# Optimization experiments

Hardware: AMD Instinct MI355X
Metric: run time of the kernel (lower is better)

Reference implementation:

```python
import jax, jax.numpy as jnp
import numpy as np

N_NODES = 100_000
N_EDGES = 1_600_000
IN_FEAT = 128
N_HEADS = 8
OUT_FEAT = 16
HF = N_HEADS * OUT_FEAT  # 128
NEG_SLOPE = 0.2


def setup_inputs() -> dict:
    key = jax.random.key(0)
    k = jax.random.split(key, 9)
    x = jax.random.normal(k[0], (N_NODES, IN_FEAT), dtype=jnp.float32)
    src = jax.random.randint(k[1], (N_EDGES,), 0, N_NODES, dtype=jnp.int64)
    dst = jax.random.randint(k[2], (N_EDGES,), 0, N_NODES, dtype=jnp.int64)
    sv = 1.0 / np.sqrt(IN_FEAT)
    sa = 1.0 / np.sqrt(HF)
    Wv = jax.random.normal(k[3], (IN_FEAT, HF), dtype=jnp.float32) * sv
    bv = jnp.zeros((HF,), dtype=jnp.float32)
    Wq = jax.random.normal(k[4], (HF, N_HEADS), dtype=jnp.float32) * sa
    bq = jnp.zeros((N_HEADS,), dtype=jnp.float32)
    Wk = jax.random.normal(k[5], (HF, N_HEADS), dtype=jnp.float32) * sa
    bk = jnp.zeros((N_HEADS,), dtype=jnp.float32)
    return {"x": x, "src": src, "dst": dst, "Wv": Wv, "bv": bv,
            "Wq": Wq, "bq": bq, "Wk": Wk, "bk": bk}


def reference(x, src, dst, Wv, bv, Wq, bq, Wk, bk):
    # Dense projections (homogeneous graph: h_src == h_dst == h)
    h = x @ Wv + bv                       # [N, H*F]
    q = h @ Wq + bq                       # [N, H]  (query, attached via dst)
    k = h @ Wk + bk                       # [N, H]  (key, attached via src)
    u = h.reshape(N_NODES, N_HEADS, OUT_FEAT)  # [N, H, F]

    # Edge scores: u_add_v('k','q') -> e_ij = k[src] + q[dst], then leaky-relu
    e = k[src] + q[dst]                   # [E, H]
    coeff = jnp.where(e >= 0, e, NEG_SLOPE * e)

    # Segment softmax over incoming edges of each destination node
    seg_max = jax.ops.segment_max(coeff, dst, num_segments=N_NODES)   # [N, H]
    ex = jnp.exp(coeff - seg_max[dst])                                # [E, H]
    denom = jax.ops.segment_sum(ex, dst, num_segments=N_NODES)       # [N, H]
    attn = ex / denom[dst]                                           # [E, H]

    # Weighted message + scatter-sum aggregate
    m = u[src] * attn[:, :, None]                                    # [E, H, F]
    v = jax.ops.segment_sum(m, dst, num_segments=N_NODES)            # [N, H, F]

    return jnp.mean(v, axis=1)                                       # [N, F]
```

## Files before the change

### kernel.cpp

```cpp
#include <hip/hip_runtime.h>
#include <hip/hip_fp16.h>

#define NFEAT 128
#define NHEADS 8
#define OUTF 16
#define NPB 256
#define MAXNB 512
#define CAP 4736

typedef _Float16 half8 __attribute__((ext_vector_type(8)));
typedef float float4v __attribute__((ext_vector_type(4)));

__global__ __launch_bounds__(256) void prep_kernel(
    const float* __restrict__ Wv, const float* __restrict__ bv,
    const float* __restrict__ Wq, const float* __restrict__ bq,
    const float* __restrict__ Wk, const float* __restrict__ bk,
    float* __restrict__ Wvq, float* __restrict__ Wvk,
    float* __restrict__ bq2, float* __restrict__ bk2)
{
    const int t = threadIdx.x;
    const int idx = blockIdx.x * 256 + t;
    const int m  = idx >> 10;
    const int j  = (idx >> 3) & 127;
    const int hd = idx & 7;
    const float* w = m ? Wk : Wq;
    float acc = 0.f;
#pragma unroll 8
    for (int c = 0; c < NFEAT; c++) acc += Wv[j * NFEAT + c] * w[c * NHEADS + hd];
    if (m) Wvk[j * NHEADS + hd] = acc;
    else   Wvq[j * NHEADS + hd] = acc;

    if (blockIdx.x == 0 && t < 16) {
        int mm = t >> 3, hh = t & 7;
        const float* ww = mm ? Wk : Wq;
        float a = mm ? bk[hh] : bq[hh];
        for (int c = 0; c < NFEAT; c++) a += bv[c] * ww[c * NHEADS + hh];
        if (mm) bk2[hh] = a;
        else    bq2[hh] = a;
    }
}

__global__ __launch_bounds__(256) void gemm_h_kernel(
    const float* __restrict__ x, const float* __restrict__ Wv,
    const float* __restrict__ bv, const float* __restrict__ Wvq,
    const float* __restrict__ Wvk, const float* __restrict__ bq2,
    const float* __restrict__ bk2, __half* __restrict__ h,
    float* __restrict__ qarr, float* __restrict__ karr, int M)
{
    __shared__ _Float16 sw[144][136];
    const int t = threadIdx.x;

    for (int i = t; i < 128 * 128; i += 256) {
        int k = i >> 7, n = i & 127;
        sw[n][k] = (_Float16)Wv[i];
    }
    for (int i = t; i < 128 * 16; i += 256) {
        int k = i >> 4, o = i & 15;
        float v = (o < 8) ? Wvq[k * 8 + o] : Wvk[k * 8 + (o - 8)];
        sw[128 + o][k] = (_Float16)v;
    }
    __syncthreads();

    const int wave = t >> 6, lane = t & 63;
    const int quad = lane >> 4, l16 = lane & 15;
    const int nstrips = (M + 15) >> 4;

    float bvv[8];
#pragma unroll
    for (int tl = 0; tl < 8; tl++) bvv[tl] = bv[tl * 16 + l16];
    const float qb = (l16 < 8) ? bq2[l16] : bk2[l16 - 8];

#pragma unroll
    for (int s = 0; s < 2; s++) {
        const int strip = blockIdx.x * 8 + wave + s * 4;
        if (strip >= nstrips) break;
        const int row0 = strip * 16;
        const int xr = row0 + l16;
        const bool ok = (xr < M);
        const float* xp = x + (size_t)xr * NFEAT + quad * 8;

        half8 af[4];
#pragma unroll
        for (int kc = 0; kc < 4; kc++) {
            float4 f0 = make_float4(0.f, 0.f, 0.f, 0.f);
            float4 f1 = make_float4(0.f, 0.f, 0.f, 0.f);
            if (ok) {
                f0 = *(const float4*)(xp + kc * 32);
                f1 = *(const float4*)(xp + kc * 32 + 4);
            }
            half8 a;
            a[0] = (_Float16)f0.x; a[1] = (_Float16)f0.y;
            a[2] = (_Float16)f0.z; a[3] = (_Float16)f0.w;
            a[4] = (_Float16)f1.x; a[5] = (_Float16)f1.y;
            a[6] = (_Float16)f1.z; a[7] = (_Float16)f1.w;
            af[kc] = a;
        }

        float4v acc[9];
#pragma unroll
        for (int tl = 0; tl < 9; tl++) acc[tl] = (float4v){0.f, 0.f, 0.f, 0.f};

#pragma unroll
        for (int kc = 0; kc < 4; kc++) {
#pragma unroll
            for (int tl = 0; tl < 9; tl++) {
                half8 b = *(const half8*)&sw[tl * 16 + l16][kc * 32 + quad * 8];
                acc[tl] = __builtin_amdgcn_mfma_f32_16x16x32_f16(af[kc], b, acc[tl], 0, 0, 0);
            }
        }

#pragma unroll
        for (int r = 0; r < 4; r++) {
            int row = row0 + quad * 4 + r;
            if (row < M) {
#pragma unroll
                for (int tl = 0; tl < 8; tl++)
                    h[(size_t)row * NFEAT + tl * 16 + l16] =
                        __float2half(acc[tl][r] + bvv[tl]);
                float qv = acc[8][r] + qb;
                if (l16 < 8) qarr[(size_t)row * NHEADS + l16] = qv;
                else         karr[(size_t)row * NHEADS + (l16 - 8)] = qv;
            }
        }
    }
}

__global__ __launch_bounds__(1024) void bin_kernel(
    const int* __restrict__ src, const int* __restrict__ dst,
    int* __restrict__ tail, int* __restrict__ bin, int E, int NB)
{
    __shared__ int lcnt[MAXNB];
    __shared__ int lbase[MAXNB];
    const int t = threadIdx.x;
    const int e0 = blockIdx.x * 8192;

    for (int i = t; i < NB; i += 1024) lcnt[i] = 0;
    __syncthreads();

    int pack[8], bkt[8], rank[8];
#pragma unroll
    for (int k = 0; k < 8; k++) {
        int e = e0 + k * 1024 + t;
        bkt[k] = -1;
        if (e < E) {
            int d = dst[e];
            pack[k] = (src[e] << 8) | (d & (NPB - 1));
            bkt[k]  = d >> 8;
            rank[k] = atomicAdd(&lcnt[bkt[k]], 1);
        }
    }
    __syncthreads();
    for (int i = t; i < NB; i += 1024)
        lbase[i] = lcnt[i] ? atomicAdd(&tail[i], lcnt[i]) : 0;
    __syncthreads();

#pragma unroll
    for (int k = 0; k < 8; k++) {
        if (bkt[k] >= 0) {
            int pos = lbase[bkt[k]] + rank[k];
            if (pos < CAP) bin[(size_t)bkt[k] * CAP + pos] = pack[k];
        }
    }
}

__global__ __launch_bounds__(1024) void bucket_build_kernel(
    const int* __restrict__ bin, const int* __restrict__ tail,
    int* __restrict__ deg, int* __restrict__ off,
    int* __restrict__ csr, int N, int NB)
{
    __shared__ int stail[MAXNB];
    __shared__ int lcnt[NPB];
    __shared__ int lcur[NPB];
    __shared__ int lcsr[CAP];

    const int b = blockIdx.x;
    const int t = threadIdx.x;

    for (int i = t; i < MAXNB; i += 1024) stail[i] = (i < NB) ? tail[i] : 0;
    if (t < NPB) lcnt[t] = 0;
    __syncthreads();

    for (int o = 1; o < MAXNB; o <<= 1) {
        int u = (t < MAXNB && t >= o) ? stail[t - o] : 0;
        __syncthreads();
        if (t < MAXNB) stail[t] += u;
        __syncthreads();
    }
    const int gbase = (b > 0) ? stail[b - 1] : 0;
    const int cnt = min(tail[b], CAP);
    const int n0 = b << 8;
    const int* mybin = bin + (size_t)b * CAP;

    for (int i = t; i < cnt; i += 1024) atomicAdd(&lcnt[mybin[i] & (NPB - 1)], 1);
    __syncthreads();

    if (t < NPB) lcur[t] = lcnt[t];
    __syncthreads();
    for (int o = 1; o < NPB; o <<= 1) {
        int u = (t < NPB && t >= o) ? lcur[t - o] : 0;
        __syncthreads();
        if (t < NPB) lcur[t] += u;
        __syncthreads();
    }
    if (t < NPB) {
        int excl = lcur[t] - lcnt[t];
        lcur[t] = excl;
        int node = n0 + t;
        if (node < N) {
            deg[node] = lcnt[t];
            off[node] = gbase + excl;
        }
    }
    __syncthreads();

    for (int i = t; i < cnt; i += 1024) {
        int p = mybin[i];
        int r = atomicAdd(&lcur[p & (NPB - 1)], 1);
        lcsr[r] = p >> 8;
    }
    __syncthreads();

    for (int i = t; i < cnt; i += 1024) csr[gbase + i] = lcsr[i];
}

__global__ __launch_bounds__(256) void agg_kernel(
    const int* __restrict__ csr, const int* __restrict__ off,
    const int* __restrict__ deg, const float* __restrict__ karr,
    const float* __restrict__ qarr, const __half* __restrict__ h,
    float* __restrict__ out, int nnodes)
{
    const int wave = threadIdx.x >> 6;
    const int lane = threadIdx.x & 63;
    const int d = blockIdx.x * 4 + wave;
    if (d >= nnodes) return;

    const int dg = deg[d];
    const int o0 = off[d];
    const int h8  = lane & 7;
    const int eg  = lane >> 4;
    const int l16 = lane & 15;
    const int hd  = l16 >> 1;
    const float q1 = qarr[d * NHEADS + h8];
    const __half* hbase = h + l16 * 8;

    __half2 acc0 = __float2half2_rn(0.f);
    __half2 acc1 = __float2half2_rn(0.f);
    __half2 acc2 = __float2half2_rn(0.f);
    __half2 acc3 = __float2half2_rn(0.f);
    float den8 = 0.f;

    for (int c0 = 0; c0 < dg; c0 += 64) {
        const int cnt = min(64, dg - c0);
        int sv = (lane < cnt) ? csr[o0 + c0 + lane] : 0;
        for (int g0 = 0; g0 < cnt; g0 += 8) {
            const int epos = g0 + (lane >> 3);
            int s8 = __shfl(sv, epos, 64);
            float p = 0.f;
            if (epos < cnt) {
                float c = karr[s8 * NHEADS + h8] + q1;
                c = fmaxf(c, 0.2f * c);
                p = __expf(c) * 0.0009765625f;
            }
            den8 += p;
            __half2 ph2 = __half2half2(__float2half(p));
            int phi = *(int*)&ph2;
#pragma unroll
            for (int i = 0; i < 2; ++i) {
                int jr  = (i << 2) + eg;
                int sl  = __shfl(sv, g0 + jr, 64);
                int pw  = __shfl(phi, (jr << 3) + hd, 64);
                __half2 pv = *(__half2*)&pw;
                float4 raw = *(const float4*)(hbase + (size_t)sl * NFEAT);
                __half2 v0 = *(__half2*)&raw.x;
                __half2 v1 = *(__half2*)&raw.y;
                __half2 v2 = *(__half2*)&raw.z;
                __half2 v3 = *(__half2*)&raw.w;
                acc0 = __hfma2(pv, v0, acc0);
                acc1 = __hfma2(pv, v1, acc1);
                acc2 = __hfma2(pv, v2, acc2);
                acc3 = __hfma2(pv, v3, acc3);
            }
        }
    }

    den8 += __shfl_xor(den8, 8, 64);
    den8 += __shfl_xor(den8, 16, 64);
    den8 += __shfl_xor(den8, 32, 64);
    float dh = __shfl(den8, hd, 64);

    float f[8];
    f[0] = __low2float(acc0); f[1] = __high2float(acc0);
    f[2] = __low2float(acc1); f[3] = __high2float(acc1);
    f[4] = __low2float(acc2); f[5] = __high2float(acc2);
    f[6] = __low2float(acc3); f[7] = __high2float(acc3);

#pragma unroll
    for (int o = 16; o <= 32; o <<= 1)
#pragma unroll
        for (int i = 0; i < 8; i++) f[i] += __shfl_xor(f[i], o, 64);

    const float inv = (dg > 0) ? 0.125f / dh : 0.f;
#pragma unroll
    for (int i = 0; i < 8; i++) f[i] *= inv;

#pragma unroll
    for (int o = 2; o <= 8; o <<= 1)
#pragma unroll
        for (int i = 0; i < 8; i++) f[i] += __shfl_xor(f[i], o, 64);

    if (lane < 2) {
        float4* o4 = (float4*)(out + (size_t)d * OUTF + lane * 8);
        o4[0] = make_float4(f[0], f[1], f[2], f[3]);
        o4[1] = make_float4(f[4], f[5], f[6], f[7]);
    }
}

extern "C" void kernel_launch(void* const* d_in, const int* in_sizes, int n_in,
                              void* d_out, int out_size, void* d_ws, size_t ws_size,
                              hipStream_t stream)
{
    const float* x   = (const float*)d_in[0];
    const int*   src = (const int*)d_in[1];
    const int*   dst = (const int*)d_in[2];
    const float* Wv  = (const float*)d_in[3];
    const float* bv  = (const float*)d_in[4];
    const float* Wq  = (const float*)d_in[5];
    const float* bq  = (const float*)d_in[6];
    const float* Wk  = (const float*)d_in[7];
    const float* bk  = (const float*)d_in[8];
    float* out = (float*)d_out;

    const int N = in_sizes[0] / NFEAT;
    const int E = in_sizes[1];
    const int NB = (N + NPB - 1) / NPB;

    __half* h   = (__half*)d_ws;
    float* qarr = (float*)d_ws + (size_t)N * (NFEAT / 2);
    float* karr = qarr + (size_t)N * NHEADS;
    int* deg    = (int*)(karr + (size_t)N * NHEADS);
    int* off    = deg + N;
    int* csr    = off + N;
    float* Wvq  = (float*)(csr + E);
    float* Wvk  = Wvq + NFEAT * NHEADS;
    float* bq2  = Wvk + NFEAT * NHEADS;
    float* bk2  = bq2 + NHEADS;
    int* tail   = (int*)(bk2 + NHEADS);
    int* bin    = tail + MAXNB;

    hipMemsetAsync(tail, 0, MAXNB * sizeof(int), stream);

    prep_kernel<<<dim3(8), dim3(256), 0, stream>>>(Wv, bv, Wq, bq, Wk, bk,
                                                   Wvq, Wvk, bq2, bk2);

    bin_kernel<<<dim3((E + 8191) / 8192), dim3(1024), 0, stream>>>(
        src, dst, tail, bin, E, NB);

    bucket_build_kernel<<<dim3(NB), dim3(1024), 0, stream>>>(
        bin, tail, deg, off, csr, N, NB);

    const int nstrips = (N + 15) / 16;
    gemm_h_kernel<<<dim3((nstrips + 7) / 8), dim3(256), 0, stream>>>(
        x, Wv, bv, Wvq, Wvk, bq2, bk2, h, qarr, karr, N);

    agg_kernel<<<dim3((N + 3) / 4), dim3(256), 0, stream>>>(
        csr, off, deg, karr, qarr, h, out, N);
}
```

Before: 237.0 us.

## Fuse GEMM and edge binning into one interleaved kernel; drop memset

Merges the MFMA projection kernel and the edge-binning kernel into a single launch where even blocks do the GEMM (16 strips each) and odd blocks bin 4096 edges with 256 threads. The tail counters are zeroed inside prep_kernel instead of by a separate memset, and bucket_build now uses 512 threads and takes bucket counts from the scanned shared array. The aim is to cut launch count and let the compute-bound GEMM overlap with the memory- and atomic-bound binning. The cost is a larger per-block register footprint, because both paths share one kernel and smem allocation.

After: 242.9 us. 1.03x slower.

```diff
diff --git a/kernel.cpp b/kernel.cpp
--- a/kernel.cpp
+++ b/kernel.cpp
@@ -16,10 +16,11 @@
     const float* __restrict__ Wq, const float* __restrict__ bq,
     const float* __restrict__ Wk, const float* __restrict__ bk,
     float* __restrict__ Wvq, float* __restrict__ Wvk,
-    float* __restrict__ bq2, float* __restrict__ bk2)
+    float* __restrict__ bq2, float* __restrict__ bk2, int* __restrict__ tail)
 {
     const int t = threadIdx.x;
     const int idx = blockIdx.x * 256 + t;
+    if (idx < MAXNB) tail[idx] = 0;
     const int m  = idx >> 10;
     const int j  = (idx >> 3) & 127;
     const int hd = idx & 7;
@@ -40,130 +41,136 @@
     }
 }
 
-__global__ __launch_bounds__(256) void gemm_h_kernel(
+__global__ __launch_bounds__(256) void k1_kernel(
     const float* __restrict__ x, const float* __restrict__ Wv,
     const float* __restrict__ bv, const float* __restrict__ Wvq,
     const float* __restrict__ Wvk, const float* __restrict__ bq2,
     const float* __restrict__ bk2, __half* __restrict__ h,
-    float* __restrict__ qarr, float* __restrict__ karr, int M)
-{
-    __shared__ _Float16 sw[144][136];
+    float* __restrict__ qarr, float* __restrict__ karr, int M,
+    const int* __restrict__ src, const int* __restrict__ dst,
+    int* __restrict__ tail, int* __restrict__ bin, int E, int NB,
+    int GB, int BB)
+{
+    __shared__ char smem[144 * 136 * 2];
+    const int bid = blockIdx.x;
     const int t = threadIdx.x;
 
-    for (int i = t; i < 128 * 128; i += 256) {
-        int k = i >> 7, n = i & 127;
-        sw[n][k] = (_Float16)Wv[i];
-    }
-    for (int i = t; i < 128 * 16; i += 256) {
-        int k = i >> 4, o = i & 15;
-        float v = (o < 8) ? Wvq[k * 8 + o] : Wvk[k * 8 + (o - 8)];
-        sw[128 + o][k] = (_Float16)v;
-    }
-    __syncthreads();
-
-    const int wave = t >> 6, lane = t & 63;
-    const int quad = lane >> 4, l16 = lane & 15;
-    const int nstrips = (M + 15) >> 4;
-
-    float bvv[8];
-#pragma unroll
-    for (int tl = 0; tl < 8; tl++) bvv[tl] = bv[tl * 16 + l16];
-    const float qb = (l16 < 8) ? bq2[l16] : bk2[l16 - 8];
-
-#pragma unroll
-    for (int s = 0; s < 2; s++) {
-        const int strip = blockIdx.x * 8 + wave + s * 4;
-        if (strip >= nstrips) break;
-        const int row0 = strip * 16;
-        const int xr = row0 + l16;
-        const bool ok = (xr < M);
-        const float* xp = x + (size_t)xr * NFEAT + quad * 8;
-
-        half8 af[4];
-#pragma unroll
-        for (int kc = 0; kc < 4; kc++) {
-            float4 f0 = make_float4(0.f, 0.f, 0.f, 0.f);
-            float4 f1 = make_float4(0.f, 0.f, 0.f, 0.f);
-            if (ok) {
-                f0 = *(const float4*)(xp + kc * 32);
-                f1 = *(const float4*)(xp + kc * 32 + 4);
-            }
-            half8 a;
-            a[0] = (_Float16)f0.x; a[1] = (_Float16)f0.y;
-            a[2] = (_Float16)f0.z; a[3] = (_Float16)f0.w;
-            a[4] = (_Float16)f1.x; a[5] = (_Float16)f1.y;
-            a[6] = (_Float16)f1.z; a[7] = (_Float16)f1.w;
-            af[kc] = a;
-        }
-
-        float4v acc[9];
-#pragma unroll
-        for (int tl = 0; tl < 9; tl++) acc[tl] = (float4v){0.f, 0.f, 0.f, 0.f};
-
-#pragma unroll
-        for (int kc = 0; kc < 4; kc++) {
-#pragma unroll
-            for (int tl = 0; tl < 9; tl++) {
-                half8 b = *(const half8*)&sw[tl * 16 + l16][kc * 32 + quad * 8];
-                acc[tl] = __builtin_amdgcn_mfma_f32_16x16x32_f16(af[kc], b, acc[tl], 0, 0, 0);
-            }
-        }
-
-#pragma unroll
-        for (int r = 0; r < 4; r++) {
-            int row = row0 + quad * 4 + r;
-            if (row < M) {
-#pragma unroll
-                for (int tl = 0; tl < 8; tl++)
-                    h[(size_t)row * NFEAT + tl * 16 + l16] =
-                        __float2half(acc[tl][r] + bvv[tl]);
-                float qv = acc[8][r] + qb;
-                if (l16 < 8) qarr[(size_t)row * NHEADS + l16] = qv;
-                else         karr[(size_t)row * NHEADS + (l16 - 8)] = qv;
-            }
-        }
-    }
-}
-
-__global__ __launch_bounds__(1024) void bin_kernel(
-    const int* __restrict__ src, const int* __restrict__ dst,
-    int* __restrict__ tail, int* __restrict__ bin, int E, int NB)
-{
-    __shared__ int lcnt[MAXNB];
-    __shared__ int lbase[MAXNB];
-    const int t = threadIdx.x;
-    const int e0 = blockIdx.x * 8192;
-
-    for (int i = t; i < NB; i += 1024) lcnt[i] = 0;
-    __syncthreads();
-
-    int pack[8], bkt[8], rank[8];
-#pragma unroll
-    for (int k = 0; k < 8; k++) {
-        int e = e0 + k * 1024 + t;
-        bkt[k] = -1;
-        if (e < E) {
-            int d = dst[e];
-            pack[k] = (src[e] << 8) | (d & (NPB - 1));
-            bkt[k]  = d >> 8;
-            rank[k] = atomicAdd(&lcnt[bkt[k]], 1);
-        }
-    }
-    __syncthreads();
-    for (int i = t; i < NB; i += 1024)
-        lbase[i] = lcnt[i] ? atomicAdd(&tail[i], lcnt[i]) : 0;
-    __syncthreads();
-
-#pragma unroll
-    for (int k = 0; k < 8; k++) {
-        if (bkt[k] >= 0) {
-            int pos = lbase[bkt[k]] + rank[k];
-            if (pos < CAP) bin[(size_t)bkt[k] * CAP + pos] = pack[k];
-        }
-    }
-}
-
-__global__ __launch_bounds__(1024) void bucket_build_kernel(
+    if ((bid & 1) == 0) {
+        const int gb = bid >> 1;
+        if (gb >= GB) return;
+        _Float16 (*sw)[136] = (_Float16(*)[136])smem;
+
+        for (int i = t; i < 128 * 128; i += 256) {
+            int k = i >> 7, n = i & 127;
+            sw[n][k] = (_Float16)Wv[i];
+        }
+        for (int i = t; i < 128 * 16; i += 256) {
+            int k = i >> 4, o = i & 15;
+            float v = (o < 8) ? Wvq[k * 8 + o] : Wvk[k * 8 + (o - 8)];
+            sw[128 + o][k] = (_Float16)v;
+        }
+        __syncthreads();
+
+        const int wave = t >> 6, lane = t & 63;
+        const int quad = lane >> 4, l16 = lane & 15;
+        const int nstrips = (M + 15) >> 4;
+
+        float bvv[8];
+#pragma unroll
+        for (int tl = 0; tl < 8; tl++) bvv[tl] = bv[tl * 16 + l16];
+        const float qb = (l16 < 8) ? bq2[l16] : bk2[l16 - 8];
+
+#pragma unroll
+        for (int s = 0; s < 4; s++) {
+            const int strip = gb * 16 + wave * 4 + s;
+            if (strip >= nstrips) break;
+            const int row0 = strip * 16;
+            const int xr = row0 + l16;
+            const bool ok = (xr < M);
+            const float* xp = x + (size_t)xr * NFEAT + quad * 8;
+
+            half8 af[4];
+#pragma unroll
+            for (int kc = 0; kc < 4; kc++) {
+                float4 f0 = make_float4(0.f, 0.f, 0.f, 0.f);
+                float4 f1 = make_float4(0.f, 0.f, 0.f, 0.f);
+                if (ok) {
+                    f0 = *(const float4*)(xp + kc * 32);
+                    f1 = *(const float4*)(xp + kc * 32 + 4);
+                }
+                half8 a;
+                a[0] = (_Float16)f0.x; a[1] = (_Float16)f0.y;
+                a[2] = (_Float16)f0.z; a[3] = (_Float16)f0.w;
+                a[4] = (_Float16)f1.x; a[5] = (_Float16)f1.y;
+                a[6] = (_Float16)f1.z; a[7] = (_Float16)f1.w;
+                af[kc] = a;
+            }
+
+            float4v acc[9];
+#pragma unroll
+            for (int tl = 0; tl < 9; tl++) acc[tl] = (float4v){0.f, 0.f, 0.f, 0.f};
+
+#pragma unroll
+            for (int kc = 0; kc < 4; kc++) {
+#pragma unroll
+                for (int tl = 0; tl < 9; tl++) {
+                    half8 b = *(const half8*)&sw[tl * 16 + l16][kc * 32 + quad * 8];
+                    acc[tl] = __builtin_amdgcn_mfma_f32_16x16x32_f16(af[kc], b, acc[tl], 0, 0, 0);
+                }
+            }
+
+#pragma unroll
+            for (int r = 0; r < 4; r++) {
+                int row = row0 + quad * 4 + r;
+                if (row < M) {
+#pragma unroll
+                    for (int tl = 0; tl < 8; tl++)
+                        h[(size_t)row * NFEAT + tl * 16 + l16] =
+                            __float2half(acc[tl][r] + bvv[tl]);
+                    float qv = acc[8][r] + qb;
+                    if (l16 < 8) qarr[(size_t)row * NHEADS + l16] = qv;
+                    else         karr[(size_t)row * NHEADS + (l16 - 8)] = qv;
+                }
+            }
+        }
+    } else {
+        const int bb = bid >> 1;
+        if (bb >= BB) return;
+        int* lcnt  = (int*)smem;
+        int* lbase = lcnt + MAXNB;
+        const int e0 = bb * 4096;
+
+        for (int i = t; i < MAXNB; i += 256) lcnt[i] = 0;
+        __syncthreads();
+
+        int pack[16], bkt[16], rank[16];
+#pragma unroll
+        for (int k = 0; k < 16; k++) {
+            int e = e0 + k * 256 + t;
+            bkt[k] = -1;
+            if (e < E) {
+                int d = dst[e];
+                pack[k] = (src[e] << 8) | (d & (NPB - 1));
+                bkt[k]  = d >> 8;
+                rank[k] = atomicAdd(&lcnt[bkt[k]], 1);
+            }
+        }
+        __syncthreads();
+        for (int i = t; i < NB; i += 256)
+            lbase[i] = lcnt[i] ? atomicAdd(&tail[i], lcnt[i]) : 0;
+        __syncthreads();
+
+#pragma unroll
+        for (int k = 0; k < 16; k++) {
+            if (bkt[k] >= 0) {
+                int pos = lbase[bkt[k]] + rank[k];
+                if (pos < CAP) bin[(size_t)bkt[k] * CAP + pos] = pack[k];
+            }
+        }
+    }
+}
+
+__global__ __launch_bounds__(512) void bucket_build_kernel(
     const int* __restrict__ bin, const int* __restrict__ tail,
     int* __restrict__ deg, int* __restrict__ off,
     int* __restrict__ csr, int N, int NB)
@@ -176,22 +183,22 @@
     const int b = blockIdx.x;
     const int t = threadIdx.x;
 
-    for (int i = t; i < MAXNB; i += 1024) stail[i] = (i < NB) ? tail[i] : 0;
+    stail[t] = (t < NB) ? tail[t] : 0;
     if (t < NPB) lcnt[t] = 0;
     __syncthreads();
 
     for (int o = 1; o < MAXNB; o <<= 1) {
-        int u = (t < MAXNB && t >= o) ? stail[t - o] : 0;
-        __syncthreads();
-        if (t < MAXNB) stail[t] += u;
+        int u = (t >= o) ? stail[t - o] : 0;
+        __syncthreads();
+        stail[t] += u;
         __syncthreads();
     }
     const int gbase = (b > 0) ? stail[b - 1] : 0;
-    const int cnt = min(tail[b], CAP);
+    const int cnt = min(stail[b] - gbase, CAP);
     const int n0 = b << 8;
     const int* mybin = bin + (size_t)b * CAP;
 
-    for (int i = t; i < cnt; i += 1024) atomicAdd(&lcnt[mybin[i] & (NPB - 1)], 1);
+    for (int i = t; i < cnt; i += 512) atomicAdd(&lcnt[mybin[i] & (NPB - 1)], 1);
     __syncthreads();
 
     if (t < NPB) lcur[t] = lcnt[t];
@@ -213,14 +220,14 @@
     }
     __syncthreads();
 
-    for (int i = t; i < cnt; i += 1024) {
+    for (int i = t; i < cnt; i += 512) {
         int p = mybin[i];
         int r = atomicAdd(&lcur[p & (NPB - 1)], 1);
         lcsr[r] = p >> 8;
     }
     __syncthreads();
 
-    for (int i = t; i < cnt; i += 1024) csr[gbase + i] = lcsr[i];
+    for (int i = t; i < cnt; i += 512) csr[gbase + i] = lcsr[i];
 }
 
 __global__ __launch_bounds__(256) void agg_kernel(
@@ -347,20 +354,19 @@
     int* tail   = (int*)(bk2 + NHEADS);
     int* bin    = tail + MAXNB;
 
-    hipMemsetAsync(tail, 0, MAXNB * sizeof(int), stream);
-
     prep_kernel<<<dim3(8), dim3(256), 0, stream>>>(Wv, bv, Wq, bq, Wk, bk,
-                                                   Wvq, Wvk, bq2, bk2);
-
-    bin_kernel<<<dim3((E + 8191) / 8192), dim3(1024), 0, stream>>>(
-        src, dst, tail, bin, E, NB);
-
-    bucket_build_kernel<<<dim3(NB), dim3(1024), 0, stream>>>(
+                                                   Wvq, Wvk, bq2, bk2, tail);
+
+    const int nstrips = (N + 15) / 16;
+    const int GB = (nstrips + 15) / 16;
+    const int BB = (E + 4095) / 4096;
+    const int grid1 = 2 * max(GB, BB);
+    k1_kernel<<<dim3(grid1), dim3(256), 0, stream>>>(
+        x, Wv, bv, Wvq, Wvk, bq2, bk2, h, qarr, karr, N,
+        src, dst, tail, bin, E, NB, GB, BB);
+
+    bucket_build_kernel<<<dim3(NB), dim3(512), 0, stream>>>(
         bin, tail, deg, off, csr, N, NB);
-
-    const int nstrips = (N + 15) / 16;
-    gemm_h_kernel<<<dim3((nstrips + 7) / 8), dim3(256), 0, stream>>>(
-        x, Wv, bv, Wvq, Wvk, bq2, bk2, h, qarr, karr, N);
 
     agg_kernel<<<dim3((N + 3) / 4), dim3(256), 0, stream>>>(
         csr, off, deg, karr, qarr, h, out, N);
```
